# Performance work log

Measured on AMD Instinct MI355X. Metric: run time of the kernel, lower is better.

Reference implementation:

```python
import jax, jax.numpy as jnp
import numpy as np

N = 50000
E = 250000
NUM_ETYPES = 4
H = 2  # num_heads
EPS = 1e-12


def _gat_conv(x, W, al, ar, b, src, dst):
    # x: (N, in_dim); W: (in_dim, H*D); al/ar/b: (H, D); src/dst: (E,)
    D = al.shape[-1]
    feat = (x @ W).reshape(-1, H, D)            # (N, H, D)
    el = jnp.sum(feat * al, axis=-1)            # (N, H)
    er = jnp.sum(feat * ar, axis=-1)            # (N, H)
    e = jax.nn.leaky_relu(el[src] + er[dst], 0.2)   # (E, H)
    emax = jax.ops.segment_max(e, dst, num_segments=N)
    ex = jnp.exp(e - emax[dst])
    denom = jax.ops.segment_sum(ex, dst, num_segments=N)
    alpha = ex / denom[dst]                     # (E, H) segment softmax over in-edges
    msg = feat[src] * alpha[:, :, None]         # (E, H, D)
    out = jax.ops.segment_sum(msg, dst, num_segments=N)  # (N, H, D)
    return out + b


def _hetero_layer(x, W, al, ar, b, edges):
    # vmap GATConv over the edge-type axis, then HeteroGraphConv aggregate='mean'
    outs = jax.vmap(lambda w, a, r, bb, e: _gat_conv(x, w, a, r, bb, e[0], e[1]))(
        W, al, ar, b, edges)                    # (T, N, H, D)
    return jnp.mean(outs, axis=0)               # (N, H, D)


def _post(v):
    # relu -> F.normalize(dim=1, i.e. across heads) -> dropout(eval: identity) -> mean over heads
    v = jax.nn.relu(v)
    norm = jnp.sqrt(jnp.sum(v * v, axis=1, keepdims=True))
    v = v / jnp.maximum(norm, EPS)
    return jnp.mean(v, axis=1)                  # (N, D)


def setup_inputs() -> dict:
    key = jax.random.key(0)
    ks = jax.random.split(key, 16)
    s = 0.05
    inp = {
        'x': jax.random.normal(ks[0], (N, 23), jnp.float32),
        'edges': jax.random.randint(ks[1], (NUM_ETYPES, 2, E), 0, N, jnp.int32),
        'W0': jax.random.normal(ks[2], (NUM_ETYPES, 23, H * 64), jnp.float32) * s,
        'al0': jax.random.normal(ks[3], (NUM_ETYPES, H, 64), jnp.float32) * s,
        'ar0': jax.random.normal(ks[4], (NUM_ETYPES, H, 64), jnp.float32) * s,
        'b0': jnp.zeros((NUM_ETYPES, H, 64), jnp.float32),
        'W1': jax.random.normal(ks[5], (NUM_ETYPES, 64, H * 64), jnp.float32) * s,
        'al1': jax.random.normal(ks[6], (NUM_ETYPES, H, 64), jnp.float32) * s,
        'ar1': jax.random.normal(ks[7], (NUM_ETYPES, H, 64), jnp.float32) * s,
        'b1': jnp.zeros((NUM_ETYPES, H, 64), jnp.float32),
        'W2': jax.random.normal(ks[8], (NUM_ETYPES, 64, H * 64), jnp.float32) * s,
        'al2': jax.random.normal(ks[9], (NUM_ETYPES, H, 64), jnp.float32) * s,
        'ar2': jax.random.normal(ks[10], (NUM_ETYPES, H, 64), jnp.float32) * s,
        'b2': jnp.zeros((NUM_ETYPES, H, 64), jnp.float32),
    }
    return inp


def reference(x, edges, W0, al0, ar0, b0, W1, al1, ar1, b1, W2, al2, ar2, b2):
    h = x  # feature_by_level, feat_level=0
    h = _post(_hetero_layer(h, W0, al0, ar0, b0, edges))
    h = _post(_hetero_layer(h, W1, al1, ar1, b1, edges))
    h = jnp.mean(_hetero_layer(h, W2, al2, ar2, b2, edges), axis=1)  # (N, out_dim)
    out = jnp.mean(h, axis=0, keepdims=True)    # dgl.mean_nodes, single graph -> (1, out_dim)
    return out
```

## Files before the change

kernel.cpp:

```cpp
#include <hip/hip_runtime.h>

#define NN 50000
#define NE 250000
#define NSCAN_BLKS ((NN + 255)/256)
#define EDGE_BLKS ((4*NE + 255)/256)
#define NBUCK 4
#define BSZ ((NN + NBUCK - 1)/NBUCK)

typedef __attribute__((ext_vector_type(8))) short bf16x8;
typedef __attribute__((ext_vector_type(4))) float f32x4;

__device__ inline ushort f2bf(float f) {
  uint u = __float_as_uint(f);
  return (ushort)((u + 0x7fffu + ((u >> 16) & 1u)) >> 16);
}
__device__ inline float bf2f(ushort b) { return __uint_as_float(((uint)b) << 16); }

__global__ __launch_bounds__(256) void zero_ints(int* __restrict__ p, int n) {
  int i = blockIdx.x*256 + threadIdx.x;
  if (i < n) p[i] = 0;
}
__global__ __launch_bounds__(256) void zero_floats(float* __restrict__ p, int n) {
  int i = blockIdx.x*256 + threadIdx.x;
  if (i < n) p[i] = 0.f;
}

__global__ __launch_bounds__(256) void count_kernel(const int* __restrict__ edges, int* __restrict__ counts) {
  int idx = blockIdx.x*256 + threadIdx.x;
  if (idx >= 4*NE) return;
  int t = idx / NE, e = idx - t*NE;
  int dst = edges[(size_t)t*2*NE + NE + e];
  atomicAdd(&counts[t*NN + dst], 1);
}

__global__ __launch_bounds__(256) void sumdeg_kernel(const int* __restrict__ counts, int* __restrict__ totdeg) {
  int v = blockIdx.x*256 + threadIdx.x;
  if (v < NN) totdeg[v] = counts[v] + counts[NN+v] + counts[2*NN+v] + counts[3*NN+v];
}

__global__ __launch_bounds__(256) void scan1_kernel(const int* __restrict__ in, int* __restrict__ out, int* __restrict__ bsum, int n) {
  __shared__ int sd[256];
  int i = blockIdx.x*256 + threadIdx.x;
  int v = (i < n) ? in[i] : 0;
  sd[threadIdx.x] = v;
  __syncthreads();
  for (int off = 1; off < 256; off <<= 1) {
    int add = (threadIdx.x >= off) ? sd[threadIdx.x - off] : 0;
    __syncthreads();
    sd[threadIdx.x] += add;
    __syncthreads();
  }
  if (i < n) out[i] = sd[threadIdx.x] - v;
  if (threadIdx.x == 255) bsum[blockIdx.x] = sd[255];
}

__global__ __launch_bounds__(1024) void scan2_kernel(int* __restrict__ bsum, int nb) {
  __shared__ int sd[1024];
  int i = threadIdx.x;
  int v = (i < nb) ? bsum[i] : 0;
  sd[i] = v;
  __syncthreads();
  for (int off = 1; off < 1024; off <<= 1) {
    int add = (i >= off) ? sd[i - off] : 0;
    __syncthreads();
    sd[i] += add;
    __syncthreads();
  }
  if (i < nb) bsum[i] = sd[i] - v;
}

__global__ __launch_bounds__(256) void scan3b_kernel(int* __restrict__ rp, const int* __restrict__ bsum, int n, int total) {
  int i = blockIdx.x*256 + threadIdx.x;
  if (i < n) rp[i] += bsum[blockIdx.x];
  if (i == 0) rp[n] = total;
}

__global__ __launch_bounds__(256) void make_cursor_kernel(const int* __restrict__ rp2, const int* __restrict__ counts,
                                                          int* __restrict__ cursor, int* __restrict__ sub_ptr) {
  int v = blockIdx.x*256 + threadIdx.x;
  if (v >= NN) return;
  int b = rp2[v];
  int s1 = b  + counts[v];
  int s2 = s1 + counts[NN+v];
  int s3 = s2 + counts[2*NN+v];
  cursor[v] = b; cursor[NN+v] = s1; cursor[2*NN+v] = s2; cursor[3*NN+v] = s3;
  sub_ptr[NN+v] = s1; sub_ptr[2*NN+v] = s2; sub_ptr[3*NN+v] = s3;
}

__global__ __launch_bounds__(256) void scatter_bucketed(const int* __restrict__ edges, int* __restrict__ cursor,
                                                        int* __restrict__ col2) {
  const int b = blockIdx.x / EDGE_BLKS;
  const int idx = (blockIdx.x - b*EDGE_BLKS)*256 + threadIdx.x;
  if (idx >= 4*NE) return;
  const int t = idx / NE, e = idx - t*NE;
  const int dst = edges[(size_t)t*2*NE + NE + e];
  if (dst < b*BSZ || dst >= (b+1)*BSZ) return;
  const int src = edges[(size_t)t*2*NE + e];
  const int pos = atomicAdd(&cursor[t*NN + dst], 1);
  col2[pos] = src;
}

__global__ __launch_bounds__(256) void convert_x_kernel(const float* __restrict__ x, ushort* __restrict__ xpad) {
  int i = blockIdx.x*256 + threadIdx.x;
  if (i >= NN*64) return;
  int k = i & 63, n = i >> 6;
  xpad[i] = (k < 23) ? f2bf(x[n*23 + k]) : (ushort)0;
}

__global__ __launch_bounds__(256) void convert_wb_kernel(const float* __restrict__ W, ushort* __restrict__ WB, int Kin) {
  int i = blockIdx.x*256 + threadIdx.x;
  if (i >= 4*128*64) return;
  int k = i & 63, c = (i >> 6) & 127, t = i >> 13;
  float w = (k < Kin) ? W[((size_t)t*Kin + k)*128 + c] : 0.f;
  WB[i] = f2bf(w);
}

__global__ __launch_bounds__(256) void walwar_kernel(const float* __restrict__ W, const float* __restrict__ al,
                                                     const float* __restrict__ ar, ushort* __restrict__ wwb, int Kin) {
  int i = blockIdx.x*256 + threadIdx.x;
  if (i >= 16*64) return;
  int c = i >> 6, k = i & 63;
  int lr = c >> 3, t = (c >> 1) & 3, h = c & 1;
  float v = 0.f;
  if (k < Kin) {
    const float* A = (lr ? ar : al) + t*128 + h*64;
    const float* wr = W + ((size_t)t*Kin + k)*128 + h*64;
    for (int d = 0; d < 64; ++d) v += wr[d]*A[d];
  }
  wwb[i] = f2bf(v);
}

__global__ __launch_bounds__(256)
void elk_kernel(const ushort* __restrict__ hbf, const ushort* __restrict__ wwb,
                float* __restrict__ elp, float* __restrict__ erp)
{
  __shared__ ushort BS[16*64];
  __shared__ float sC[16*66];
  const int tid = threadIdx.x;
  if (tid < 128) ((bf16x8*)BS)[tid] = ((const bf16x8*)wwb)[tid];
  __syncthreads();

  const int wv = tid >> 6, lane = tid & 63;
  const int mrow = lane & 15, kq = lane >> 4;
  const int anode = blockIdx.x*64 + wv*16 + mrow;

  const bf16x8 a0 = *(const bf16x8*)(hbf + (size_t)anode*64 + kq*8);
  const bf16x8 a1 = *(const bf16x8*)(hbf + (size_t)anode*64 + 32 + kq*8);
  const bf16x8 b0 = *(const bf16x8*)(BS + mrow*64 + kq*8);
  const bf16x8 b1 = *(const bf16x8*)(BS + mrow*64 + 32 + kq*8);

  f32x4 acc = (f32x4){0.f,0.f,0.f,0.f};
  acc = __builtin_amdgcn_mfma_f32_16x16x32_bf16(a0, b0, acc, 0, 0, 0);
  acc = __builtin_amdgcn_mfma_f32_16x16x32_bf16(a1, b1, acc, 0, 0, 0);

  #pragma unroll
  for (int r = 0; r < 4; ++r) sC[mrow*66 + wv*16 + kq*4 + r] = acc[r];
  __syncthreads();

  const int t = tid >> 6, n = tid & 63;
  const int node = blockIdx.x*64 + n;
  if (node < NN) {
    float2 e2 = make_float2(sC[(t*2+0)*66 + n], sC[(t*2+1)*66 + n]);
    float2 r2 = make_float2(sC[(8+t*2+0)*66 + n], sC[(8+t*2+1)*66 + n]);
    ((float2*)elp)[(size_t)t*NN + node] = e2;
    ((float2*)erp)[(size_t)t*NN + node] = r2;
  }
}

__global__ __launch_bounds__(256)
void gather_kernel(const ushort* __restrict__ hbf, const float* __restrict__ elp,
                   const float* __restrict__ erp, const int* __restrict__ col2,
                   const int* __restrict__ row_ptr2, const int* __restrict__ sub_ptr,
                   ushort* __restrict__ agg)
{
  const int v = __builtin_amdgcn_readfirstlane(blockIdx.x*4 + (threadIdx.x >> 6));
  const int lane = threadIdx.x & 63;
  const int h2 = lane >> 5;
  const int j  = lane & 31;
  const uint* hb32 = (const uint*)hbf;
  uint* agg32 = (uint*)agg;

  const int b0 = row_ptr2[v];
  const int b4 = row_ptr2[v+1];
  const int s1 = sub_ptr[NN+v], s2 = sub_ptr[2*NN+v], s3 = sub_ptr[3*NN+v];
  const int bounds[5] = {b0, s1, s2, s3, b4};

  #pragma unroll
  for (int t = 0; t < 4; ++t) {
    const int lo = bounds[t], hi = bounds[t+1];
    float ox = 0.f, oy = 0.f;
    if (lo < hi) {
      const float2 er2 = ((const float2*)erp)[(size_t)t*NN + v];
      float sum0 = 0.f, sum1 = 0.f, tx0 = 0.f, ty0 = 0.f, tx1 = 0.f, ty1 = 0.f;
      #pragma unroll 2
      for (int q = lo + h2; q < hi; q += 2) {
        const int src = col2[q];
        const float2 e2 = ((const float2*)elp)[(size_t)t*NN + src];
        float u0 = e2.x + er2.x, u1 = e2.y + er2.y;
        u0 = (u0 > 0.f) ? u0 : 0.2f*u0;
        u1 = (u1 > 0.f) ? u1 : 0.2f*u1;
        const float p0 = __expf(fminf(u0, 80.f));
        const float p1 = __expf(fminf(u1, 80.f));
        sum0 += p0; sum1 += p1;
        const uint w = hb32[(uint)src*32u + (uint)j];
        const float xv0 = __uint_as_float(w << 16);
        const float xv1 = __uint_as_float(w & 0xffff0000u);
        tx0 += p0*xv0; ty0 += p0*xv1;
        tx1 += p1*xv0; ty1 += p1*xv1;
      }
      sum0 += __shfl_xor(sum0, 32); sum1 += __shfl_xor(sum1, 32);
      tx0 += __shfl_xor(tx0, 32);   ty0 += __shfl_xor(ty0, 32);
      tx1 += __shfl_xor(tx1, 32);   ty1 += __shfl_xor(ty1, 32);
      const float i0 = __builtin_amdgcn_rcpf(sum0);
      const float i1 = __builtin_amdgcn_rcpf(sum1);
      ox = h2 ? tx1*i1 : tx0*i0;
      oy = h2 ? ty1*i1 : ty0*i0;
    }
    const uint pk = (uint)f2bf(ox) | ((uint)f2bf(oy) << 16);
    __builtin_nontemporal_store(pk, &agg32[(size_t)(t*NN + v)*64 + h2*32 + j]);
  }
}

__global__ __launch_bounds__(256)
void transform_kernel(const ushort* __restrict__ agg, const ushort* __restrict__ WB,
                      const float* __restrict__ ball, ushort* __restrict__ hout, int post)
{
  __shared__ ushort WT[2*128*64];
  __shared__ float sb[128];
  const int tid = threadIdx.x;
  if (tid < 128) sb[tid] = 0.25f*(ball[tid] + ball[128+tid] + ball[256+tid] + ball[384+tid]);

  const int wv = tid >> 6, lane = tid & 63;
  const int mrow = lane & 15, kq = lane >> 4;
  const int node0 = blockIdx.x*64;
  const int anode = node0 + wv*16 + mrow;

  f32x4 acc[8];
  #pragma unroll
  for (int nb = 0; nb < 8; ++nb) acc[nb] = (f32x4){0.f,0.f,0.f,0.f};

  for (int tb = 0; tb < 4; tb += 2) {
    __syncthreads();
    for (int i = tid; i < 2048; i += 256) {
      int row = i >> 3, jj = i & 7;
      bf16x8 val = ((const bf16x8*)WB)[tb*1024 + i];
      *(bf16x8*)((char*)WT + row*128 + ((jj ^ (row & 7))*16)) = val;
    }
    __syncthreads();
    #pragma unroll
    for (int t2 = 0; t2 < 2; ++t2) {
      const int t = tb + t2;
      const ushort* ar_ = agg + ((size_t)t*NN + anode)*128;
      const bf16x8 a00 = __builtin_nontemporal_load((const bf16x8*)(ar_ + kq*8));
      const bf16x8 a01 = __builtin_nontemporal_load((const bf16x8*)(ar_ + 32 + kq*8));
      const bf16x8 a10 = __builtin_nontemporal_load((const bf16x8*)(ar_ + 64 + kq*8));
      const bf16x8 a11 = __builtin_nontemporal_load((const bf16x8*)(ar_ + 96 + kq*8));
      #pragma unroll
      for (int nb = 0; nb < 8; ++nb) {
        const int row = t2*128 + nb*16 + mrow;
        const bf16x8 b0 = *(const bf16x8*)((const char*)WT + row*128 + ((kq       ^ (row&7))*16));
        const bf16x8 b1 = *(const bf16x8*)((const char*)WT + row*128 + (((4 + kq) ^ (row&7))*16));
        acc[nb] = __builtin_amdgcn_mfma_f32_16x16x32_bf16(nb < 4 ? a00 : a10, b0, acc[nb], 0, 0, 0);
        acc[nb] = __builtin_amdgcn_mfma_f32_16x16x32_bf16(nb < 4 ? a01 : a11, b1, acc[nb], 0, 0, 0);
      }
    }
  }

  const int noder = node0 + wv*16 + kq*4;
  #pragma unroll
  for (int nb = 0; nb < 4; ++nb) {
    const int d = nb*16 + mrow;
    const float bm0 = sb[d], bm1 = sb[64 + d];
    #pragma unroll
    for (int r = 0; r < 4; ++r) {
      if (noder + r < NN) {
        float h0 = 0.25f*acc[nb][r]   + bm0;
        float h1 = 0.25f*acc[nb+4][r] + bm1;
        float o;
        if (post) {
          h0 = fmaxf(h0, 0.f); h1 = fmaxf(h1, 0.f);
          o = 0.5f*(h0 + h1) / fmaxf(sqrtf(h0*h0 + h1*h1), 1e-12f);
        } else {
          o = 0.5f*(h0 + h1);
        }
        hout[(size_t)(noder + r)*64 + d] = f2bf(o);
      }
    }
  }
}

__global__ __launch_bounds__(256) void reduce_nodes(const ushort* __restrict__ hn, float* __restrict__ accum) {
  __shared__ float sd[256];
  int d = threadIdx.x & 63, rg = threadIdx.x >> 6;
  float s = 0.f;
  for (int r = blockIdx.x*4 + rg; r < NN; r += gridDim.x*4) s += bf2f(hn[(size_t)r*64 + d]);
  sd[threadIdx.x] = s;
  __syncthreads();
  if (threadIdx.x < 64) {
    s = sd[threadIdx.x] + sd[threadIdx.x+64] + sd[threadIdx.x+128] + sd[threadIdx.x+192];
    atomicAdd(&accum[threadIdx.x], s);
  }
}
__global__ __launch_bounds__(64) void final_out_kernel(const float* __restrict__ accum, float* __restrict__ out) {
  int d = threadIdx.x;
  if (d < 64) out[d] = accum[d] * (1.0f/NN);
}

extern "C" void kernel_launch(void* const* d_in, const int* in_sizes, int n_in,
                              void* d_out, int out_size, void* d_ws, size_t ws_size,
                              hipStream_t stream) {
  const float* x     = (const float*)d_in[0];
  const int*   edges = (const int*)d_in[1];
  const float* W[3]  = {(const float*)d_in[2], (const float*)d_in[6], (const float*)d_in[10]};
  const float* al[3] = {(const float*)d_in[3], (const float*)d_in[7], (const float*)d_in[11]};
  const float* ar[3] = {(const float*)d_in[4], (const float*)d_in[8], (const float*)d_in[12]};
  const float* b[3]  = {(const float*)d_in[5], (const float*)d_in[9], (const float*)d_in[13]};

  char* ws = (char*)d_ws;
  auto up = [](size_t x_) { return (x_ + 255) & ~(size_t)255; };

  const size_t szAgg  = ((size_t)4*NN + 64)*128*sizeof(ushort);
  const size_t szElp  = (size_t)4*NN*2*sizeof(float);
  const size_t szHB   = (size_t)(NN+64)*64*sizeof(ushort);
  const size_t szWB   = (size_t)4*128*64*sizeof(ushort);
  const size_t szWWB  = (size_t)16*64*sizeof(ushort);
  const size_t szCol  = (size_t)4*NE*sizeof(int);
  const size_t szI4   = (size_t)4*NN*sizeof(int);
  const size_t szI1   = (size_t)(NN+1)*sizeof(int);

  size_t o = 0;
  ushort* agg    = (ushort*)(ws + o); o += up(szAgg);
  float*  elp    = (float*)(ws + o);  o += up(szElp);
  float*  erp    = (float*)(ws + o);  o += up(szElp);
  ushort* xpad   = (ushort*)(ws + o); o += up(szHB);
  ushort* hbuf   = (ushort*)(ws + o); o += up(szHB);
  ushort* WB     = (ushort*)(ws + o); o += up(szWB);
  ushort* wwb    = (ushort*)(ws + o); o += up(szWWB);
  float*  accum  = (float*)(ws + o);  o += up(256);
  int*    col2   = (int*)(ws + o);    o += up(szCol);
  int* row_ptr2  = (int*)(ws + o);    o += up(szI1);
  int* totdeg    = (int*)(ws + o);    o += up(szI1);
  int* cursor    = (int*)(ws + o);    o += up(szI4);
  int* counts    = (int*)(ws + o);    o += up(szI4);
  int* sub_ptr   = (int*)(ws + o);    o += up(szI4);
  int* bsum      = (int*)(ws + o);    o += up(4096);

  zero_ints<<<(4*NN + 255)/256, 256, 0, stream>>>(counts, 4*NN);
  count_kernel<<<EDGE_BLKS, 256, 0, stream>>>(edges, counts);
  sumdeg_kernel<<<NSCAN_BLKS, 256, 0, stream>>>(counts, totdeg);
  scan1_kernel<<<NSCAN_BLKS, 256, 0, stream>>>(totdeg, row_ptr2, bsum, NN);
  scan2_kernel<<<1, 1024, 0, stream>>>(bsum, NSCAN_BLKS);
  scan3b_kernel<<<NSCAN_BLKS, 256, 0, stream>>>(row_ptr2, bsum, NN, 4*NE);
  make_cursor_kernel<<<NSCAN_BLKS, 256, 0, stream>>>(row_ptr2, counts, cursor, sub_ptr);
  scatter_bucketed<<<NBUCK*EDGE_BLKS, 256, 0, stream>>>(edges, cursor, col2);

  convert_x_kernel<<<(NN*64 + 255)/256, 256, 0, stream>>>(x, xpad);

  const int gemmGX = (NN + 63)/64;

  for (int l = 0; l < 3; ++l) {
    const ushort* hin = (l == 0) ? xpad : hbuf;
    const int Kin = (l == 0) ? 23 : 64;
    convert_wb_kernel<<<(4*128*64 + 255)/256, 256, 0, stream>>>(W[l], WB, Kin);
    walwar_kernel<<<(16*64 + 255)/256, 256, 0, stream>>>(W[l], al[l], ar[l], wwb, Kin);
    elk_kernel<<<gemmGX, 256, 0, stream>>>(hin, wwb, elp, erp);
    gather_kernel<<<NN/4, 256, 0, stream>>>(hin, elp, erp, col2, row_ptr2, sub_ptr, agg);
    transform_kernel<<<gemmGX, 256, 0, stream>>>(agg, WB, b[l], hbuf, (l < 2) ? 1 : 0);
  }

  zero_floats<<<1, 64, 0, stream>>>(accum, 64);
  reduce_nodes<<<256, 256, 0, stream>>>(hbuf, accum);
  final_out_kernel<<<1, 64, 0, stream>>>(accum, (float*)d_out);
}
```

Before: 396.7 us.

## Hoist weight prep out of layer loop, bucket count pass, drop LDS staging in transform

The per-layer weight conversion and attention-vector folding kernels become single launches that handle all three layers up front, cutting four kernel launches. The degree count pass now uses the same destination-bucketed scheme as the scatter, so its atomics stay within a smaller address range, at the cost of reading the edge array four times. The transform kernel no longer stages weights in swizzled shared memory with barriers and instead loads B fragments straight from global memory through cache, and it computes the bias mean per thread rather than in shared memory.

```diff
diff --git a/kernel.cpp b/kernel.cpp
--- a/kernel.cpp
+++ b/kernel.cpp
@@ -25,11 +25,13 @@
   if (i < n) p[i] = 0.f;
 }
 
-__global__ __launch_bounds__(256) void count_kernel(const int* __restrict__ edges, int* __restrict__ counts) {
-  int idx = blockIdx.x*256 + threadIdx.x;
+__global__ __launch_bounds__(256) void count_bucketed(const int* __restrict__ edges, int* __restrict__ counts) {
+  const int b = blockIdx.x / EDGE_BLKS;
+  const int idx = (blockIdx.x - b*EDGE_BLKS)*256 + threadIdx.x;
   if (idx >= 4*NE) return;
-  int t = idx / NE, e = idx - t*NE;
-  int dst = edges[(size_t)t*2*NE + NE + e];
+  const int t = idx / NE, e = idx - t*NE;
+  const int dst = edges[(size_t)t*2*NE + NE + e];
+  if (dst < b*BSZ || dst >= (b+1)*BSZ) return;
   atomicAdd(&counts[t*NN + dst], 1);
 }
 
@@ -107,27 +109,39 @@
   xpad[i] = (k < 23) ? f2bf(x[n*23 + k]) : (ushort)0;
 }
 
-__global__ __launch_bounds__(256) void convert_wb_kernel(const float* __restrict__ W, ushort* __restrict__ WB, int Kin) {
-  int i = blockIdx.x*256 + threadIdx.x;
-  if (i >= 4*128*64) return;
-  int k = i & 63, c = (i >> 6) & 127, t = i >> 13;
+__global__ __launch_bounds__(256) void convert_wb3_kernel(const float* __restrict__ W0, const float* __restrict__ W1,
+                                                          const float* __restrict__ W2, ushort* __restrict__ WB3) {
+  int i = blockIdx.x*256 + threadIdx.x;
+  if (i >= 3*4*128*64) return;
+  int l = i / (4*128*64); int r = i - l*(4*128*64);
+  int k = r & 63, c = (r >> 6) & 127, t = r >> 13;
+  const float* W = (l == 0) ? W0 : (l == 1) ? W1 : W2;
+  const int Kin = (l == 0) ? 23 : 64;
   float w = (k < Kin) ? W[((size_t)t*Kin + k)*128 + c] : 0.f;
-  WB[i] = f2bf(w);
-}
-
-__global__ __launch_bounds__(256) void walwar_kernel(const float* __restrict__ W, const float* __restrict__ al,
-                                                     const float* __restrict__ ar, ushort* __restrict__ wwb, int Kin) {
-  int i = blockIdx.x*256 + threadIdx.x;
-  if (i >= 16*64) return;
-  int c = i >> 6, k = i & 63;
+  WB3[i] = f2bf(w);
+}
+
+__global__ __launch_bounds__(256) void walwar3_kernel(const float* __restrict__ W0, const float* __restrict__ W1,
+                                                      const float* __restrict__ W2, const float* __restrict__ al0,
+                                                      const float* __restrict__ al1, const float* __restrict__ al2,
+                                                      const float* __restrict__ ar0, const float* __restrict__ ar1,
+                                                      const float* __restrict__ ar2, ushort* __restrict__ wwb3) {
+  int i = blockIdx.x*256 + threadIdx.x;
+  if (i >= 3*16*64) return;
+  int l = i / (16*64); int r = i - l*(16*64);
+  int c = r >> 6, k = r & 63;
   int lr = c >> 3, t = (c >> 1) & 3, h = c & 1;
+  const float* W  = (l == 0) ? W0 : (l == 1) ? W1 : W2;
+  const float* al = (l == 0) ? al0 : (l == 1) ? al1 : al2;
+  const float* ar = (l == 0) ? ar0 : (l == 1) ? ar1 : ar2;
+  const int Kin = (l == 0) ? 23 : 64;
   float v = 0.f;
   if (k < Kin) {
     const float* A = (lr ? ar : al) + t*128 + h*64;
     const float* wr = W + ((size_t)t*Kin + k)*128 + h*64;
     for (int d = 0; d < 64; ++d) v += wr[d]*A[d];
   }
-  wwb[i] = f2bf(v);
+  wwb3[i] = f2bf(v);
 }
 
 __global__ __launch_bounds__(256)
@@ -225,11 +239,7 @@
 void transform_kernel(const ushort* __restrict__ agg, const ushort* __restrict__ WB,
                       const float* __restrict__ ball, ushort* __restrict__ hout, int post)
 {
-  __shared__ ushort WT[2*128*64];
-  __shared__ float sb[128];
   const int tid = threadIdx.x;
-  if (tid < 128) sb[tid] = 0.25f*(ball[tid] + ball[128+tid] + ball[256+tid] + ball[384+tid]);
-
   const int wv = tid >> 6, lane = tid & 63;
   const int mrow = lane & 15, kq = lane >> 4;
   const int node0 = blockIdx.x*64;
@@ -239,30 +249,21 @@
   #pragma unroll
   for (int nb = 0; nb < 8; ++nb) acc[nb] = (f32x4){0.f,0.f,0.f,0.f};
 
-  for (int tb = 0; tb < 4; tb += 2) {
-    __syncthreads();
-    for (int i = tid; i < 2048; i += 256) {
-      int row = i >> 3, jj = i & 7;
-      bf16x8 val = ((const bf16x8*)WB)[tb*1024 + i];
-      *(bf16x8*)((char*)WT + row*128 + ((jj ^ (row & 7))*16)) = val;
-    }
-    __syncthreads();
+  #pragma unroll
+  for (int t = 0; t < 4; ++t) {
+    const ushort* ar_ = agg + ((size_t)t*NN + anode)*128;
+    const bf16x8 a00 = __builtin_nontemporal_load((const bf16x8*)(ar_ + kq*8));
+    const bf16x8 a01 = __builtin_nontemporal_load((const bf16x8*)(ar_ + 32 + kq*8));
+    const bf16x8 a10 = __builtin_nontemporal_load((const bf16x8*)(ar_ + 64 + kq*8));
+    const bf16x8 a11 = __builtin_nontemporal_load((const bf16x8*)(ar_ + 96 + kq*8));
+    const ushort* wb_t = WB + (size_t)t*128*64;
     #pragma unroll
-    for (int t2 = 0; t2 < 2; ++t2) {
-      const int t = tb + t2;
-      const ushort* ar_ = agg + ((size_t)t*NN + anode)*128;
-      const bf16x8 a00 = __builtin_nontemporal_load((const bf16x8*)(ar_ + kq*8));
-      const bf16x8 a01 = __builtin_nontemporal_load((const bf16x8*)(ar_ + 32 + kq*8));
-      const bf16x8 a10 = __builtin_nontemporal_load((const bf16x8*)(ar_ + 64 + kq*8));
-      const bf16x8 a11 = __builtin_nontemporal_load((const bf16x8*)(ar_ + 96 + kq*8));
-      #pragma unroll
-      for (int nb = 0; nb < 8; ++nb) {
-        const int row = t2*128 + nb*16 + mrow;
-        const bf16x8 b0 = *(const bf16x8*)((const char*)WT + row*128 + ((kq       ^ (row&7))*16));
-        const bf16x8 b1 = *(const bf16x8*)((const char*)WT + row*128 + (((4 + kq) ^ (row&7))*16));
-        acc[nb] = __builtin_amdgcn_mfma_f32_16x16x32_bf16(nb < 4 ? a00 : a10, b0, acc[nb], 0, 0, 0);
-        acc[nb] = __builtin_amdgcn_mfma_f32_16x16x32_bf16(nb < 4 ? a01 : a11, b1, acc[nb], 0, 0, 0);
-      }
+    for (int nb = 0; nb < 8; ++nb) {
+      const int c = nb*16 + mrow;
+      const bf16x8 b0 = *(const bf16x8*)(wb_t + c*64 + kq*8);
+      const bf16x8 b1 = *(const bf16x8*)(wb_t + c*64 + 32 + kq*8);
+      acc[nb] = __builtin_amdgcn_mfma_f32_16x16x32_bf16(nb < 4 ? a00 : a10, b0, acc[nb], 0, 0, 0);
+      acc[nb] = __builtin_amdgcn_mfma_f32_16x16x32_bf16(nb < 4 ? a01 : a11, b1, acc[nb], 0, 0, 0);
     }
   }
 
@@ -270,7 +271,8 @@
   #pragma unroll
   for (int nb = 0; nb < 4; ++nb) {
     const int d = nb*16 + mrow;
-    const float bm0 = sb[d], bm1 = sb[64 + d];
+    const float bm0 = 0.25f*(ball[d]      + ball[128+d]      + ball[256+d]      + ball[384+d]);
+    const float bm1 = 0.25f*(ball[64+d]   + ball[192+d]      + ball[320+d]      + ball[448+d]);
     #pragma unroll
     for (int r = 0; r < 4; ++r) {
       if (noder + r < NN) {
@@ -322,8 +324,8 @@
   const size_t szAgg  = ((size_t)4*NN + 64)*128*sizeof(ushort);
   const size_t szElp  = (size_t)4*NN*2*sizeof(float);
   const size_t szHB   = (size_t)(NN+64)*64*sizeof(ushort);
-  const size_t szWB   = (size_t)4*128*64*sizeof(ushort);
-  const size_t szWWB  = (size_t)16*64*sizeof(ushort);
+  const size_t szWB3  = (size_t)3*4*128*64*sizeof(ushort);
+  const size_t szWWB3 = (size_t)3*16*64*sizeof(ushort);
   const size_t szCol  = (size_t)4*NE*sizeof(int);
   const size_t szI4   = (size_t)4*NN*sizeof(int);
   const size_t szI1   = (size_t)(NN+1)*sizeof(int);
@@ -334,8 +336,8 @@
   float*  erp    = (float*)(ws + o);  o += up(szElp);
   ushort* xpad   = (ushort*)(ws + o); o += up(szHB);
   ushort* hbuf   = (ushort*)(ws + o); o += up(szHB);
-  ushort* WB     = (ushort*)(ws + o); o += up(szWB);
-  ushort* wwb    = (ushort*)(ws + o); o += up(szWWB);
+  ushort* WB3    = (ushort*)(ws + o); o += up(szWB3);
+  ushort* wwb3   = (ushort*)(ws + o); o += up(szWWB3);
   float*  accum  = (float*)(ws + o);  o += up(256);
   int*    col2   = (int*)(ws + o);    o += up(szCol);
   int* row_ptr2  = (int*)(ws + o);    o += up(szI1);
@@ -345,8 +347,13 @@
   int* sub_ptr   = (int*)(ws + o);    o += up(szI4);
   int* bsum      = (int*)(ws + o);    o += up(4096);
 
+  convert_wb3_kernel<<<(3*4*128*64 + 255)/256, 256, 0, stream>>>(W[0], W[1], W[2], WB3);
+  walwar3_kernel<<<(3*16*64 + 255)/256, 256, 0, stream>>>(W[0], W[1], W[2], al[0], al[1], al[2],
+                                                          ar[0], ar[1], ar[2], wwb3);
+  convert_x_kernel<<<(NN*64 + 255)/256, 256, 0, stream>>>(x, xpad);
+
   zero_ints<<<(4*NN + 255)/256, 256, 0, stream>>>(counts, 4*NN);
-  count_kernel<<<EDGE_BLKS, 256, 0, stream>>>(edges, counts);
+  count_bucketed<<<NBUCK*EDGE_BLKS, 256, 0, stream>>>(edges, counts);
   sumdeg_kernel<<<NSCAN_BLKS, 256, 0, stream>>>(counts, totdeg);
   scan1_kernel<<<NSCAN_BLKS, 256, 0, stream>>>(totdeg, row_ptr2, bsum, NN);
   scan2_kernel<<<1, 1024, 0, stream>>>(bsum, NSCAN_BLKS);
@@ -354,15 +361,12 @@
   make_cursor_kernel<<<NSCAN_BLKS, 256, 0, stream>>>(row_ptr2, counts, cursor, sub_ptr);
   scatter_bucketed<<<NBUCK*EDGE_BLKS, 256, 0, stream>>>(edges, cursor, col2);
 
-  convert_x_kernel<<<(NN*64 + 255)/256, 256, 0, stream>>>(x, xpad);
-
   const int gemmGX = (NN + 63)/64;
 
   for (int l = 0; l < 3; ++l) {
     const ushort* hin = (l == 0) ? xpad : hbuf;
-    const int Kin = (l == 0) ? 23 : 64;
-    convert_wb_kernel<<<(4*128*64 + 255)/256, 256, 0, stream>>>(W[l], WB, Kin);
-    walwar_kernel<<<(16*64 + 255)/256, 256, 0, stream>>>(W[l], al[l], ar[l], wwb, Kin);
+    const ushort* WB  = WB3 + (size_t)l*4*128*64;
+    const ushort* wwb = wwb3 + (size_t)l*16*64;
     elk_kernel<<<gemmGX, 256, 0, stream>>>(hin, wwb, elp, erp);
     gather_kernel<<<NN/4, 256, 0, stream>>>(hin, elp, erp, col2, row_ptr2, sub_ptr, agg);
     transform_kernel<<<gemmGX, 256, 0, stream>>>(agg, WB, b[l], hbuf, (l < 2) ? 1 : 0);
```

Measured after the change: 458.5 us. 15.6% more time.
